# Kernel tuning notes

Measured on AMD Instinct MI355X. Metric: run time of the kernel, lower is better.

The kernel has to match this reference:

```python
import jax, jax.numpy as jnp
import numpy as np

NUM_CODES = 512
DIM = 64
B, M = 32, 64


def setup_inputs() -> dict:
    key = jax.random.key(0)
    k1, k2 = jax.random.split(key)
    inputs = jax.random.normal(k1, (B, M, M, DIM), dtype=jnp.float32)
    # keras 'uniform' initializer is U(-0.05, 0.05)
    embeddings = jax.random.uniform(k2, (NUM_CODES, DIM), dtype=jnp.float32,
                                    minval=-0.05, maxval=0.05)
    return {"inputs": inputs, "embeddings": embeddings}


def reference(inputs, embeddings):
    l2_inputs = jnp.sum(inputs * inputs, axis=-1, keepdims=True)      # [B,M,M,1]
    l2_embeddings = jnp.sum(embeddings * embeddings, axis=-1)          # [K]
    dot = jnp.einsum('bhwd,kd->bhwk', inputs, embeddings)              # [B,M,M,K]
    distance = l2_inputs + l2_embeddings - 2.0 * dot                   # [B,M,M,K]
    codes = jnp.argmin(distance, axis=-1).astype(jnp.int32)            # [B,M,M]
    code_vecs = embeddings[codes]                                      # [B,M,M,D]
    return codes, code_vecs
```

## Files before the change

### kernel.cpp

```cpp
#include <hip/hip_runtime.h>

#define NUM_CODES 512
#define DIM 64
#define NPIX (32 * 64 * 64)
#define BLK 512
#define NGRP 4
#define PPB 256
#define CTH 16

typedef __attribute__((ext_vector_type(8))) short bf16x8;
typedef __attribute__((ext_vector_type(4))) float f32x4;

__device__ __forceinline__ unsigned short f2bf(float f) {
    unsigned u = __float_as_uint(f);
    return (unsigned short)((u + 0x7fffu + ((u >> 16) & 1u)) >> 16);
}
__device__ __forceinline__ float bf2f(unsigned short h) {
    return __uint_as_float(((unsigned)h) << 16);
}

__global__ __launch_bounds__(256) void prep_kernel(
    const float* __restrict__ emb, unsigned short* __restrict__ AH,
    unsigned short* __restrict__ ALO, float* __restrict__ l2e,
    float* __restrict__ l2eh) {
    const int t = blockIdx.x * 256 + threadIdx.x;
    const int e0 = t * 4;
    const int c = e0 >> 6, d0 = e0 & 63;
    const float4 v = *(const float4*)(emb + c * DIM + d0);
    float f[4] = {v.x, v.y, v.z, v.w};
    unsigned short h[4], l[4];
#pragma unroll
    for (int i = 0; i < 4; ++i) {
        h[i] = f2bf(f[i]);
        l[i] = f2bf(f[i] - bf2f(h[i]));
    }
    const int ct = c >> 4, mr = c & 15, s = d0 >> 5, q = (d0 & 31) >> 3,
              j0 = d0 & 7;
    const int base = ((ct * 2 + s) * 64 + (q * 16 + mr)) * 8 + j0;
    *(ushort4*)(AH + base) = make_ushort4(h[0], h[1], h[2], h[3]);
    *(ushort4*)(ALO + base) = make_ushort4(l[0], l[1], l[2], l[3]);

    if (t < NUM_CODES) {
        const float* e = emb + t * DIM;
        float r[8];
#pragma unroll
        for (int j = 0; j < 8; ++j) {
            float w = e[j];
            r[j] = w * w;
        }
#pragma unroll
        for (int i = 8; i < DIM; i += 8)
#pragma unroll
            for (int j = 0; j < 8; ++j) {
                float w = e[i + j];
                r[j] += w * w;
            }
        float sv =
            ((r[0] + r[1]) + (r[2] + r[3])) + ((r[4] + r[5]) + (r[6] + r[7]));
        l2e[t] = sv;
        l2eh[t] = 0.5f * sv;
    }
}

__global__ __launch_bounds__(BLK, 2) void vq_main(
    const float* __restrict__ x_in, const unsigned short* __restrict__ AH,
    const unsigned short* __restrict__ ALO, const float* __restrict__ l2e,
    const float* __restrict__ l2eh, const float* __restrict__ emb,
    float* __restrict__ codes_out, float* __restrict__ vecs_out) {
    __shared__ float s_l2eh[NUM_CODES];
    __shared__ float s_l2ex[NUM_CODES];
    __shared__ float s_d1h[2][PPB];
    __shared__ float s_d2h[2][PPB];
    __shared__ int s_k1h[2][PPB];
    __shared__ int s_k2h[2][PPB];
    __shared__ float s_dbuf[PPB];
    __shared__ int s_code[PPB];

    const int tid = threadIdx.x, lane = tid & 63, wave = tid >> 6;
    const int wgrp = wave & 3, whalf = wave >> 2;
    s_l2eh[tid] = l2eh[tid];
    s_l2ex[tid] = l2e[tid];
    __syncthreads();

    const int p = lane & 15, q = lane >> 4;
    const int pw = blockIdx.x * PPB + wgrp * (16 * NGRP);

    bf16x8 bh0[NGRP], bl0[NGRP], bh1[NGRP], bl1[NGRP];
#pragma unroll
    for (int g = 0; g < NGRP; ++g) {
        const float* xb = x_in + (size_t)(pw + g * 16 + p) * DIM + q * 8;
        float4 u0 = *(const float4*)(xb);
        float4 u1 = *(const float4*)(xb + 4);
        float4 u2 = *(const float4*)(xb + 32);
        float4 u3 = *(const float4*)(xb + 36);
        float f0[8] = {u0.x, u0.y, u0.z, u0.w, u1.x, u1.y, u1.z, u1.w};
        float f1[8] = {u2.x, u2.y, u2.z, u2.w, u3.x, u3.y, u3.z, u3.w};
#pragma unroll
        for (int j = 0; j < 8; ++j) {
            unsigned short hh = f2bf(f0[j]);
            bh0[g][j] = (short)hh;
            bl0[g][j] = (short)f2bf(f0[j] - bf2f(hh));
            unsigned short h2 = f2bf(f1[j]);
            bh1[g][j] = (short)h2;
            bl1[g][j] = (short)f2bf(f1[j] - bf2f(h2));
        }
    }

    const int rowbase = q * 4;
    float d1[NGRP], d2[NGRP];
    int k1[NGRP], k2[NGRP];
#pragma unroll
    for (int g = 0; g < NGRP; ++g) {
        d1[g] = 3.4e38f;
        d2[g] = 3.4e38f;
        k1[g] = 0;
        k2[g] = 0;
    }

    const unsigned short* pAH = AH + lane * 8;
    const unsigned short* pAL = ALO + lane * 8;
    for (int ct = 0; ct < CTH; ++ct) {
        const int gt = whalf * CTH + ct;
        const bf16x8 a0h = *(const bf16x8*)(pAH + gt * 1024);
        const bf16x8 a0l = *(const bf16x8*)(pAL + gt * 1024);
        const bf16x8 a1h = *(const bf16x8*)(pAH + gt * 1024 + 512);
        const bf16x8 a1l = *(const bf16x8*)(pAL + gt * 1024 + 512);
        const int kb = gt * 16 + rowbase;
        float l2v[4];
#pragma unroll
        for (int r = 0; r < 4; ++r) l2v[r] = s_l2eh[kb + r];

#pragma unroll
        for (int g = 0; g < NGRP; ++g) {
            f32x4 acc = {0.f, 0.f, 0.f, 0.f};
            acc = __builtin_amdgcn_mfma_f32_16x16x32_bf16(a0h, bh0[g], acc, 0, 0, 0);
            acc = __builtin_amdgcn_mfma_f32_16x16x32_bf16(a1h, bh1[g], acc, 0, 0, 0);
            acc = __builtin_amdgcn_mfma_f32_16x16x32_bf16(a0l, bh0[g], acc, 0, 0, 0);
            acc = __builtin_amdgcn_mfma_f32_16x16x32_bf16(a1l, bh1[g], acc, 0, 0, 0);
            acc = __builtin_amdgcn_mfma_f32_16x16x32_bf16(a0h, bl0[g], acc, 0, 0, 0);
            acc = __builtin_amdgcn_mfma_f32_16x16x32_bf16(a1h, bl1[g], acc, 0, 0, 0);

#pragma unroll
            for (int r = 0; r < 4; ++r) {
                const float d = l2v[r] - acc[r];
                const int kk = kb + r;
                const bool c = d < d1[g], c2 = d < d2[g];
                const float nd2 = c2 ? d : d2[g];
                const int nk2 = c2 ? kk : k2[g];
                d2[g] = c ? d1[g] : nd2;
                k2[g] = c ? k1[g] : nk2;
                k1[g] = c ? kk : k1[g];
                d1[g] = c ? d : d1[g];
            }
        }
    }

#pragma unroll
    for (int g = 0; g < NGRP; ++g) {
        float a1 = d1[g], a2 = d2[g];
        int b1 = k1[g], b2 = k2[g];
#pragma unroll
        for (int off = 16; off <= 32; off <<= 1) {
            const float od1 = __shfl_xor(a1, off);
            const int ok1 = __shfl_xor(b1, off);
            const float od2 = __shfl_xor(a2, off);
            const int ok2 = __shfl_xor(b2, off);
            const bool c = od1 < a1;
            const float w1 = c ? od1 : a1;
            const int wk1 = c ? ok1 : b1;
            const float l1 = c ? a1 : od1;
            const int lk1 = c ? b1 : ok1;
            const bool cm = od2 < a2;
            const float m2 = cm ? od2 : a2;
            const int mk2 = cm ? ok2 : b2;
            const bool c3 = m2 < l1;
            a2 = c3 ? m2 : l1;
            b2 = c3 ? mk2 : lk1;
            a1 = w1;
            b1 = wk1;
        }
        if (lane < 16) {
            const int pb = wgrp * 64 + g * 16 + lane;
            s_d1h[whalf][pb] = a1;
            s_k1h[whalf][pb] = b1;
            s_d2h[whalf][pb] = a2;
            s_k2h[whalf][pb] = b2;
        }
    }
    __syncthreads();

    const int pp = tid & 255;
    const int pix = blockIdx.x * PPB + pp;
    int ka, kb;
    {
        const float d1a = s_d1h[0][pp], d1b = s_d1h[1][pp];
        const float d2a = s_d2h[0][pp], d2b = s_d2h[1][pp];
        const int k1a = s_k1h[0][pp], k1b = s_k1h[1][pp];
        const int k2a = s_k2h[0][pp], k2b = s_k2h[1][pp];
        const bool bw = d1b < d1a;
        const int bestk = bw ? k1b : k1a;
        const float w2 = bw ? d2b : d2a;
        const int wk2 = bw ? k2b : k2a;
        const float lo1 = bw ? d1a : d1b;
        const int lok1 = bw ? k1a : k1b;
        const bool c2 = (w2 < lo1) || (w2 == lo1 && wk2 < lok1);
        const int k2nd = c2 ? wk2 : lok1;
        ka = bestk;
        kb = k2nd;
        if (kb < ka) {
            const int t = ka;
            ka = kb;
            kb = t;
        }
    }
    {
        const int myk = (tid < 256) ? ka : kb;
        const float* xr = x_in + (size_t)pix * DIM;
        float x[DIM];
#pragma unroll
        for (int jj = 0; jj < 16; ++jj) {
            const float4 v = *(const float4*)(xr + jj * 4);
            x[4 * jj + 0] = v.x;
            x[4 * jj + 1] = v.y;
            x[4 * jj + 2] = v.z;
            x[4 * jj + 3] = v.w;
        }
        float r[8];
#pragma unroll
        for (int j = 0; j < 8; ++j) r[j] = x[j] * x[j];
#pragma unroll
        for (int i = 8; i < DIM; i += 8)
#pragma unroll
            for (int j = 0; j < 8; ++j) r[j] += x[i + j] * x[i + j];
        const float l2x =
            ((r[0] + r[1]) + (r[2] + r[3])) + ((r[4] + r[5]) + (r[6] + r[7]));

        const float* er = emb + (size_t)myk * DIM;
        float acc = 0.f;
#pragma unroll
        for (int d = 0; d < DIM; ++d) acc = __builtin_fmaf(x[d], er[d], acc);
        const float dist = (l2x + s_l2ex[myk]) - 2.0f * acc;
        if (tid >= 256) s_dbuf[pp] = dist;
        __syncthreads();
        if (tid < 256) {
            const float da = dist;
            const float db = s_dbuf[pp];
            const int sel = (db < da) ? kb : ka;
            s_code[pp] = sel;
            codes_out[pix] = (float)sel;
        }
    }
    __syncthreads();

    const float4* emb4 = (const float4*)emb;
    float4* vout4 = (float4*)(vecs_out + (size_t)blockIdx.x * PPB * DIM);
#pragma unroll
    for (int it = 0; it < (PPB * DIM / 4) / BLK; ++it) {
        const int fidx = tid + it * BLK;
        const int ppx = fidx >> 4, dd = fidx & 15;
        vout4[fidx] = emb4[(size_t)s_code[ppx] * (DIM / 4) + dd];
    }
}

extern "C" void kernel_launch(void* const* d_in, const int* in_sizes, int n_in,
                              void* d_out, int out_size, void* d_ws,
                              size_t ws_size, hipStream_t stream) {
    const float* x_in = (const float*)d_in[0];
    const float* emb = (const float*)d_in[1];

    unsigned short* AH = (unsigned short*)d_ws;
    unsigned short* ALO = AH + NUM_CODES * DIM;
    float* l2e = (float*)(ALO + NUM_CODES * DIM);
    float* l2eh = l2e + NUM_CODES;

    float* codes_out = (float*)d_out;
    float* vecs_out = (float*)d_out + NPIX;

    hipLaunchKernelGGL(prep_kernel, dim3(32), dim3(256), 0, stream, emb, AH,
                       ALO, l2e, l2eh);
    hipLaunchKernelGGL(vq_main, dim3(NPIX / PPB), dim3(BLK), 0, stream, x_in,
                       AH, ALO, l2e, l2eh, emb, codes_out, vecs_out);
}
```

Baseline: 137.5 us.

## Stage codebook tiles in shared memory per phase and raise occupancy target

Codebook hi/lo bf16 fragments are no longer read by every wave straight from global memory. The block now loads them cooperatively into a 32KB LDS buffer in four phases, each covering four code tiles per half, and the MFMA loop reads its fragments from LDS. Launch bounds move from 2 to 4 blocks per CU. The intent is to cut redundant global/L2 traffic and raise occupancy, at the cost of two barriers per phase, more LDS use, and tighter register limits that may cause spills.

```diff
diff --git a/kernel.cpp b/kernel.cpp
--- a/kernel.cpp
+++ b/kernel.cpp
@@ -6,7 +6,8 @@
 #define BLK 512
 #define NGRP 4
 #define PPB 256
-#define CTH 16
+#define NPH 4
+#define LTPP 4
 
 typedef __attribute__((ext_vector_type(8))) short bf16x8;
 typedef __attribute__((ext_vector_type(4))) float f32x4;
@@ -62,11 +63,12 @@
     }
 }
 
-__global__ __launch_bounds__(BLK, 2) void vq_main(
-    const float* __restrict__ x_in, const unsigned short* __restrict__ AH,
-    const unsigned short* __restrict__ ALO, const float* __restrict__ l2e,
+__global__ __launch_bounds__(BLK, 4) void vq_main(
+    const float* __restrict__ x_in, const uint4* __restrict__ AH4,
+    const uint4* __restrict__ ALO4, const float* __restrict__ l2e,
     const float* __restrict__ l2eh, const float* __restrict__ emb,
     float* __restrict__ codes_out, float* __restrict__ vecs_out) {
+    __shared__ uint4 s_A4[32 * 64];
     __shared__ float s_l2eh[NUM_CODES];
     __shared__ float s_l2ex[NUM_CODES];
     __shared__ float s_d1h[2][PPB];
@@ -80,7 +82,6 @@
     const int wgrp = wave & 3, whalf = wave >> 2;
     s_l2eh[tid] = l2eh[tid];
     s_l2ex[tid] = l2e[tid];
-    __syncthreads();
 
     const int p = lane & 15, q = lane >> 4;
     const int pw = blockIdx.x * PPB + wgrp * (16 * NGRP);
@@ -117,40 +118,58 @@
         k2[g] = 0;
     }
 
-    const unsigned short* pAH = AH + lane * 8;
-    const unsigned short* pAL = ALO + lane * 8;
-    for (int ct = 0; ct < CTH; ++ct) {
-        const int gt = whalf * CTH + ct;
-        const bf16x8 a0h = *(const bf16x8*)(pAH + gt * 1024);
-        const bf16x8 a0l = *(const bf16x8*)(pAL + gt * 1024);
-        const bf16x8 a1h = *(const bf16x8*)(pAH + gt * 1024 + 512);
-        const bf16x8 a1l = *(const bf16x8*)(pAL + gt * 1024 + 512);
-        const int kb = gt * 16 + rowbase;
-        float l2v[4];
-#pragma unroll
-        for (int r = 0; r < 4; ++r) l2v[r] = s_l2eh[kb + r];
-
-#pragma unroll
-        for (int g = 0; g < NGRP; ++g) {
-            f32x4 acc = {0.f, 0.f, 0.f, 0.f};
-            acc = __builtin_amdgcn_mfma_f32_16x16x32_bf16(a0h, bh0[g], acc, 0, 0, 0);
-            acc = __builtin_amdgcn_mfma_f32_16x16x32_bf16(a1h, bh1[g], acc, 0, 0, 0);
-            acc = __builtin_amdgcn_mfma_f32_16x16x32_bf16(a0l, bh0[g], acc, 0, 0, 0);
-            acc = __builtin_amdgcn_mfma_f32_16x16x32_bf16(a1l, bh1[g], acc, 0, 0, 0);
-            acc = __builtin_amdgcn_mfma_f32_16x16x32_bf16(a0h, bl0[g], acc, 0, 0, 0);
-            acc = __builtin_amdgcn_mfma_f32_16x16x32_bf16(a1h, bl1[g], acc, 0, 0, 0);
-
-#pragma unroll
-            for (int r = 0; r < 4; ++r) {
-                const float d = l2v[r] - acc[r];
-                const int kk = kb + r;
-                const bool c = d < d1[g], c2 = d < d2[g];
-                const float nd2 = c2 ? d : d2[g];
-                const int nk2 = c2 ? kk : k2[g];
-                d2[g] = c ? d1[g] : nd2;
-                k2[g] = c ? k1[g] : nk2;
-                k1[g] = c ? kk : k1[g];
-                d1[g] = c ? d : d1[g];
+    for (int ph = 0; ph < NPH; ++ph) {
+        __syncthreads();
+#pragma unroll
+        for (int i = 0; i < 4; ++i) {
+            const int idx = i * 512 + tid;
+            const int chunk = idx >> 6;
+            const int within = idx & 63;
+            const int hilo = chunk & 1;
+            const int s = (chunk >> 1) & 1;
+            const int lt = (chunk >> 2) & 3;
+            const int hh = (chunk >> 4) & 1;
+            const int gt = hh * 16 + ph * LTPP + lt;
+            const uint4* src = hilo ? ALO4 : AH4;
+            s_A4[idx] = src[(gt * 2 + s) * 64 + within];
+        }
+        __syncthreads();
+
+#pragma unroll
+        for (int lt = 0; lt < LTPP; ++lt) {
+            const int cb = ((whalf * 4 + lt) * 2) * 2 * 64;
+            const bf16x8 a0h = *(const bf16x8*)&s_A4[cb + lane];
+            const bf16x8 a0l = *(const bf16x8*)&s_A4[cb + 64 + lane];
+            const bf16x8 a1h = *(const bf16x8*)&s_A4[cb + 128 + lane];
+            const bf16x8 a1l = *(const bf16x8*)&s_A4[cb + 192 + lane];
+            const int gt = whalf * 16 + ph * LTPP + lt;
+            const int kb = gt * 16 + rowbase;
+            float l2v[4];
+#pragma unroll
+            for (int r = 0; r < 4; ++r) l2v[r] = s_l2eh[kb + r];
+
+#pragma unroll
+            for (int g = 0; g < NGRP; ++g) {
+                f32x4 acc = {0.f, 0.f, 0.f, 0.f};
+                acc = __builtin_amdgcn_mfma_f32_16x16x32_bf16(a0h, bh0[g], acc, 0, 0, 0);
+                acc = __builtin_amdgcn_mfma_f32_16x16x32_bf16(a1h, bh1[g], acc, 0, 0, 0);
+                acc = __builtin_amdgcn_mfma_f32_16x16x32_bf16(a0l, bh0[g], acc, 0, 0, 0);
+                acc = __builtin_amdgcn_mfma_f32_16x16x32_bf16(a1l, bh1[g], acc, 0, 0, 0);
+                acc = __builtin_amdgcn_mfma_f32_16x16x32_bf16(a0h, bl0[g], acc, 0, 0, 0);
+                acc = __builtin_amdgcn_mfma_f32_16x16x32_bf16(a1h, bl1[g], acc, 0, 0, 0);
+
+#pragma unroll
+                for (int r = 0; r < 4; ++r) {
+                    const float d = l2v[r] - acc[r];
+                    const int kk = kb + r;
+                    const bool c = d < d1[g], c2 = d < d2[g];
+                    const float nd2 = c2 ? d : d2[g];
+                    const int nk2 = c2 ? kk : k2[g];
+                    d2[g] = c ? d1[g] : nd2;
+                    k2[g] = c ? k1[g] : nk2;
+                    k1[g] = c ? kk : k1[g];
+                    d1[g] = c ? d : d1[g];
+                }
             }
         }
     }
@@ -279,5 +298,6 @@
     hipLaunchKernelGGL(prep_kernel, dim3(32), dim3(256), 0, stream, emb, AH,
                        ALO, l2e, l2eh);
     hipLaunchKernelGGL(vq_main, dim3(NPIX / PPB), dim3(BLK), 0, stream, x_in,
-                       AH, ALO, l2e, l2eh, emb, codes_out, vecs_out);
-}
+                       (const uint4*)AH, (const uint4*)ALO, l2e, l2eh, emb,
+                       codes_out, vecs_out);
+}
```

New measurement: 200.9 us. +46.0%, slower.
